# Optimization experiments

Hardware: AMD Instinct MI355X
Metric: run time of the kernel (lower is better)

## Reference

```python
import jax, jax.numpy as jnp
import numpy as np

N_QUBITS = 10
DIM = 1 << N_QUBITS  # 1024
N_OUT = 10


def _apply_ry(state, theta, q):
    # RY(theta) on qubit q; state: [B, 2^n] real (circuit is real-valued)
    B = state.shape[0]
    left = 1 << q
    right = 1 << (N_QUBITS - q - 1)
    s = state.reshape(B, left, 2, right)
    c = jnp.cos(theta / 2)
    sn = jnp.sin(theta / 2)
    s0 = c * s[:, :, 0] - sn * s[:, :, 1]
    s1 = sn * s[:, :, 0] + c * s[:, :, 1]
    return jnp.stack([s0, s1], axis=2).reshape(B, DIM)


def _apply_cnot(state, q):
    # CNOT with control q, target q+1 (adjacent, as in the source)
    B = state.shape[0]
    left = 1 << q
    right = 1 << (N_QUBITS - q - 2)
    s = state.reshape(B, left, 2, 2, right)
    s = jnp.concatenate([s[:, :, :1], jnp.flip(s[:, :, 1:], axis=3)], axis=2)
    return s.reshape(B, DIM)


def _simulate(x, params):
    B = x.shape[0]
    depth = params.shape[0]
    # weights = pi * tanh(weights)
    w = jnp.pi * jnp.tanh(params)
    # AmplitudeEmbedding: pad 784 -> 1024 with zeros, L2-normalize
    xp = jnp.pad(x, ((0, 0), (0, DIM - x.shape[1])))
    state = xp / jnp.linalg.norm(xp, axis=1, keepdims=True)
    for l in range(depth):
        # CNot(0, n): pairs (0,1),(2,3),...; CNot(1, n): pairs (1,2),(3,4),...
        for start in (0, 1):
            for i in range(start, N_QUBITS - 1, 2):
                state = _apply_cnot(state, i)
        # Rotation(w): RY(w[i]) on each wire
        for i in range(N_QUBITS):
            state = _apply_ry(state, w[l, i], i)
    # Measure: expval(PauliZ(p)) for p in range(out)
    probs = (state * state).reshape((B,) + (2,) * N_QUBITS)
    outs = []
    for p in range(N_OUT):
        axes = tuple(k + 1 for k in range(N_QUBITS) if k != p)
        marg = probs.sum(axis=axes)  # [B, 2]
        outs.append(marg[:, 0] - marg[:, 1])
    return jnp.stack(outs, axis=1).astype(jnp.float32)  # [B, out]


def setup_inputs() -> dict:
    key = jax.random.key(0)
    k1, k2 = jax.random.split(key)
    x = jax.random.uniform(k1, (16384, 784), dtype=jnp.float32)
    params = jax.random.normal(k2, (8, 10), dtype=jnp.float32)
    return {"input": x, "params": params}


def reference(input, params):
    return _simulate(input, params)
```

## Files before the change

kernel.cpp:

```cpp
#include <hip/hip_runtime.h>
#include <math.h>


template<int CTRL>
__device__ __forceinline__ float dpp_mov(float x) {
  int i = __builtin_bit_cast(int, x);
  i = __builtin_amdgcn_update_dpp(i, i, CTRL, 0xf, 0xf, true);
  return __builtin_bit_cast(float, i);
}
__device__ __forceinline__ float xl1(float x) { return dpp_mov<0xB1>(x); }
__device__ __forceinline__ float xl2(float x) { return dpp_mov<0x4E>(x); }
__device__ __forceinline__ float xl8(float x) { return dpp_mov<0x128>(x); }
template<int PAT>
__device__ __forceinline__ float swz(float x) {
  int i = __builtin_amdgcn_ds_swizzle(__builtin_bit_cast(int, x), PAT);
  return __builtin_bit_cast(float, i);
}
__device__ __forceinline__ float xl4(float x)  { return swz<0x101F>(x); }
__device__ __forceinline__ float xl16(float x) { return swz<0x401F>(x); }
__device__ __forceinline__ float bperm(int addr, float x) {
  int i = __builtin_amdgcn_ds_bpermute(addr, __builtin_bit_cast(int, x));
  return __builtin_bit_cast(float, i);
}
__device__ __forceinline__ float red32(float x) {
  x += xl1(x); x += xl2(x); x += xl4(x); x += xl8(x); x += xl16(x); return x;
}

template<int M>
__device__ __forceinline__ void ry_reg(float* v, float c, float s) {
  #pragma unroll
  for (int r = 0; r < 32; ++r) {
    if ((r & M) == 0) {
      float s0 = v[r], s1 = v[r + M];
      v[r]     = fmaf(c, s0, -(s * s1));
      v[r + M] = fmaf(s, s0,  c * s1);
    }
  }
}

template<int L2>
__device__ __forceinline__ float tree_level(float* v) {
  float a = 0.f, b = 0.f;
  #pragma unroll
  for (int j = 0; j < L2; ++j) {
    float e = v[2 * j], o = v[2 * j + 1];
    if (j & 1) b += e - o; else a += e - o;
    v[j] = e + o;
  }
  return a + b;
}

__global__ __launch_bounds__(256, 6) void circuit_kernel(
    const float* __restrict__ x, const float* __restrict__ params,
    float* __restrict__ out) {
  __shared__ float csh[160];

  const int tid  = threadIdx.x;
  const int wv   = tid >> 6;
  const int lane = tid & 63;
  const int h    = lane >> 5;
  const int l5   = lane & 31;
  const long elem = (long)blockIdx.x * 8 + wv * 2 + h;

  if (tid < 80) {
    float th = 1.57079632679489662f * tanhf(params[tid]);
    csh[2 * tid]     = cosf(th);
    csh[2 * tid + 1] = sinf(th);
  }

  int m = l5 ^ ((l5 & 4) >> 1);
  m ^= (m & 16) >> 1;
  m ^= (m & 2) >> 1;
  m ^= (m & 8) >> 1;
  const int addrE = ((lane & 32) | m) << 2;
  const int addrO = addrE ^ 64;

  float v[32];
  const float* xb = x + elem * 784 + l5;
  #pragma unroll
  for (int k = 0; k < 24; ++k) v[k] = xb[k * 32];
  v[24] = (l5 < 16) ? xb[768] : 0.f;
  #pragma unroll
  for (int k = 25; k < 32; ++k) v[k] = 0.f;

  float nn = 0.f;
  #pragma unroll
  for (int k = 0; k < 25; ++k) nn = fmaf(v[k], v[k], nn);
  nn = red32(nn);
  float scl = 1.0f / sqrtf(nn);
  #pragma unroll
  for (int k = 0; k < 25; ++k) v[k] *= scl;

  __syncthreads();

  #pragma unroll
  for (int l = 0; l < 8; ++l) {
    #pragma unroll
    for (int r = 0; r < 32; ++r) if ((r & 24) == 16) { float t = v[r]; v[r] = v[r + 8]; v[r + 8] = t; }
    #pragma unroll
    for (int r = 0; r < 32; ++r) if ((r & 6) == 4) { float t = v[r]; v[r] = v[r + 2]; v[r + 2] = t; }

    #pragma unroll
    for (int r = 0; r < 32; r += 2) {
      v[r]     = bperm(addrE, v[r]);
      v[r + 1] = bperm(addrO, v[r + 1]);
    }

    #pragma unroll
    for (int r = 0; r < 32; ++r) if ((r & 12) == 8) { float t = v[r]; v[r] = v[r + 4]; v[r + 4] = t; }
    #pragma unroll
    for (int r = 0; r < 32; ++r) if ((r & 3) == 2) { float t = v[r]; v[r] = v[r + 1]; v[r + 1] = t; }

    const float* cl = &csh[l * 20];
    ry_reg<16>(v, cl[0],  cl[1]);
    ry_reg< 8>(v, cl[2],  cl[3]);
    ry_reg< 4>(v, cl[4],  cl[5]);
    ry_reg< 2>(v, cl[6],  cl[7]);
    ry_reg< 1>(v, cl[8],  cl[9]);
    {
      float c = cl[10], s = cl[11];
      float sn = (lane & 16) ? s : -s;
      #pragma unroll
      for (int r = 0; r < 32; ++r) { float p = xl16(v[r]); v[r] = fmaf(c, v[r], sn * p); }
    }
    {
      float c = cl[12], s = cl[13];
      float sn = (lane & 8) ? s : -s;
      #pragma unroll
      for (int r = 0; r < 32; ++r) { float p = xl8(v[r]); v[r] = fmaf(c, v[r], sn * p); }
    }
    {
      float c = cl[14], s = cl[15];
      float sn = (lane & 4) ? s : -s;
      #pragma unroll
      for (int r = 0; r < 32; ++r) { float p = xl4(v[r]); v[r] = fmaf(c, v[r], sn * p); }
    }
    {
      float c = cl[16], s = cl[17];
      float sn = (lane & 2) ? s : -s;
      #pragma unroll
      for (int r = 0; r < 32; ++r) { float p = xl2(v[r]); v[r] = fmaf(c, v[r], sn * p); }
    }
    {
      float c = cl[18], s = cl[19];
      float sn = (lane & 1) ? s : -s;
      #pragma unroll
      for (int r = 0; r < 32; ++r) { float p = xl1(v[r]); v[r] = fmaf(c, v[r], sn * p); }
    }
  }

  float z[10];
  #pragma unroll
  for (int r = 0; r < 32; ++r) v[r] *= v[r];
  z[4] = red32(tree_level<16>(v));
  z[3] = red32(tree_level< 8>(v));
  z[2] = red32(tree_level< 4>(v));
  z[1] = red32(tree_level< 2>(v));
  z[0] = red32(tree_level< 1>(v));
  float W = v[0];
  { float u = W + xl1(W); u += xl2(u); u += xl4(u); u += xl8(u);  float t = u - xl16(u); z[5] = (lane & 16) ? -t : t; }
  { float u = W + xl1(W); u += xl2(u); u += xl4(u); u += xl16(u); float t = u - xl8(u);  z[6] = (lane & 8)  ? -t : t; }
  { float u = W + xl1(W); u += xl2(u); u += xl8(u); u += xl16(u); float t = u - xl4(u);  z[7] = (lane & 4)  ? -t : t; }
  { float u = W + xl1(W); u += xl4(u); u += xl8(u); u += xl16(u); float t = u - xl2(u);  z[8] = (lane & 2)  ? -t : t; }
  { float u = W + xl2(W); u += xl4(u); u += xl8(u); u += xl16(u); float t = u - xl1(u);  z[9] = (lane & 1)  ? -t : t; }

  float o = z[0];
  #pragma unroll
  for (int j = 1; j < 10; ++j) o = (l5 == j) ? z[j] : o;
  if (l5 < 10) out[elem * 10 + l5] = o;
}

extern "C" void kernel_launch(void* const* d_in, const int* in_sizes, int n_in,
                              void* d_out, int out_size, void* d_ws, size_t ws_size,
                              hipStream_t stream) {
  const float* x      = (const float*)d_in[0];
  const float* params = (const float*)d_in[1];
  float* out          = (float*)d_out;
  (void)d_ws; (void)ws_size; (void)in_sizes; (void)n_in; (void)out_size;
  circuit_kernel<<<2048, 256, 0, stream>>>(x, params, out);
}
```

Before: 73.84 us.

## Pack state into float2 vectors for packed FMA and defer normalization

```diff
diff --git a/kernel.cpp b/kernel.cpp
--- a/kernel.cpp
+++ b/kernel.cpp
@@ -1,6 +1,8 @@
 #include <hip/hip_runtime.h>
 #include <math.h>
 
+
+typedef float v2f __attribute__((ext_vector_type(2)));
 
 template<int CTRL>
 __device__ __forceinline__ float dpp_mov(float x) {
@@ -26,26 +28,14 @@
   x += xl1(x); x += xl2(x); x += xl4(x); x += xl8(x); x += xl16(x); return x;
 }
 
-template<int M>
-__device__ __forceinline__ void ry_reg(float* v, float c, float s) {
-  #pragma unroll
-  for (int r = 0; r < 32; ++r) {
-    if ((r & M) == 0) {
-      float s0 = v[r], s1 = v[r + M];
-      v[r]     = fmaf(c, s0, -(s * s1));
-      v[r + M] = fmaf(s, s0,  c * s1);
-    }
-  }
-}
-
 template<int L2>
-__device__ __forceinline__ float tree_level(float* v) {
+__device__ __forceinline__ float tree_level(float* t) {
   float a = 0.f, b = 0.f;
   #pragma unroll
   for (int j = 0; j < L2; ++j) {
-    float e = v[2 * j], o = v[2 * j + 1];
+    float e = t[2 * j], o = t[2 * j + 1];
     if (j & 1) b += e - o; else a += e - o;
-    v[j] = e + o;
+    t[j] = e + o;
   }
   return a + b;
 }
@@ -75,89 +65,134 @@
   const int addrE = ((lane & 32) | m) << 2;
   const int addrO = addrE ^ 64;
 
-  float v[32];
+  v2f w[16];
   const float* xb = x + elem * 784 + l5;
   #pragma unroll
-  for (int k = 0; k < 24; ++k) v[k] = xb[k * 32];
-  v[24] = (l5 < 16) ? xb[768] : 0.f;
-  #pragma unroll
-  for (int k = 25; k < 32; ++k) v[k] = 0.f;
-
-  float nn = 0.f;
-  #pragma unroll
-  for (int k = 0; k < 25; ++k) nn = fmaf(v[k], v[k], nn);
-  nn = red32(nn);
-  float scl = 1.0f / sqrtf(nn);
-  #pragma unroll
-  for (int k = 0; k < 25; ++k) v[k] *= scl;
+  for (int u = 0; u < 12; ++u) {
+    w[u].x = xb[u * 64];
+    w[u].y = xb[u * 64 + 32];
+  }
+  w[12].x = (l5 < 16) ? xb[768] : 0.f;
+  w[12].y = 0.f;
+  #pragma unroll
+  for (int u = 13; u < 16; ++u) w[u] = (v2f){0.f, 0.f};
+
+  v2f acc = {0.f, 0.f};
+  #pragma unroll
+  for (int u = 0; u < 13; ++u) acc += w[u] * w[u];
+  float nn  = red32(acc.x + acc.y);
+  float inv = 1.0f / nn;
 
   __syncthreads();
 
   #pragma unroll
   for (int l = 0; l < 8; ++l) {
-    #pragma unroll
-    for (int r = 0; r < 32; ++r) if ((r & 24) == 16) { float t = v[r]; v[r] = v[r + 8]; v[r + 8] = t; }
-    #pragma unroll
-    for (int r = 0; r < 32; ++r) if ((r & 6) == 4) { float t = v[r]; v[r] = v[r + 2]; v[r + 2] = t; }
-
-    #pragma unroll
-    for (int r = 0; r < 32; r += 2) {
-      v[r]     = bperm(addrE, v[r]);
-      v[r + 1] = bperm(addrO, v[r + 1]);
+    const float* cl = &csh[l * 20];
+
+    #pragma unroll
+    for (int u = 0; u < 16; ++u) if ((u & 12) == 8) { v2f t = w[u]; w[u] = w[u + 4]; w[u + 4] = t; }
+    #pragma unroll
+    for (int u = 0; u < 16; ++u) if ((u & 3) == 2) { v2f t = w[u]; w[u] = w[u + 1]; w[u + 1] = t; }
+
+    #pragma unroll
+    for (int u = 0; u < 16; ++u) {
+      w[u].x = bperm(addrE, w[u].x);
+      w[u].y = bperm(addrO, w[u].y);
     }
 
     #pragma unroll
-    for (int r = 0; r < 32; ++r) if ((r & 12) == 8) { float t = v[r]; v[r] = v[r + 4]; v[r + 4] = t; }
-    #pragma unroll
-    for (int r = 0; r < 32; ++r) if ((r & 3) == 2) { float t = v[r]; v[r] = v[r + 1]; v[r + 1] = t; }
-
-    const float* cl = &csh[l * 20];
-    ry_reg<16>(v, cl[0],  cl[1]);
-    ry_reg< 8>(v, cl[2],  cl[3]);
-    ry_reg< 4>(v, cl[4],  cl[5]);
-    ry_reg< 2>(v, cl[6],  cl[7]);
-    ry_reg< 1>(v, cl[8],  cl[9]);
-    {
-      float c = cl[10], s = cl[11];
-      float sn = (lane & 16) ? s : -s;
-      #pragma unroll
-      for (int r = 0; r < 32; ++r) { float p = xl16(v[r]); v[r] = fmaf(c, v[r], sn * p); }
-    }
-    {
-      float c = cl[12], s = cl[13];
-      float sn = (lane & 8) ? s : -s;
-      #pragma unroll
-      for (int r = 0; r < 32; ++r) { float p = xl8(v[r]); v[r] = fmaf(c, v[r], sn * p); }
-    }
-    {
-      float c = cl[14], s = cl[15];
-      float sn = (lane & 4) ? s : -s;
-      #pragma unroll
-      for (int r = 0; r < 32; ++r) { float p = xl4(v[r]); v[r] = fmaf(c, v[r], sn * p); }
-    }
-    {
-      float c = cl[16], s = cl[17];
-      float sn = (lane & 2) ? s : -s;
-      #pragma unroll
-      for (int r = 0; r < 32; ++r) { float p = xl2(v[r]); v[r] = fmaf(c, v[r], sn * p); }
-    }
-    {
-      float c = cl[18], s = cl[19];
-      float sn = (lane & 1) ? s : -s;
-      #pragma unroll
-      for (int r = 0; r < 32; ++r) { float p = xl1(v[r]); v[r] = fmaf(c, v[r], sn * p); }
-    }
-  }
-
+    for (int u = 0; u < 16; ++u) if ((u & 6) == 4) { v2f t = w[u]; w[u] = w[u + 2]; w[u + 2] = t; }
+    #pragma unroll
+    for (int u = 1; u < 16; u += 2) w[u] = __builtin_shufflevector(w[u], w[u], 1, 0);
+
+    { v2f cc = {cl[0], cl[0]}, ss = {cl[1], cl[1]};
+      #pragma unroll
+      for (int u = 0; u < 16; ++u) if ((u & 8) == 0) {
+        v2f a = w[u], b = w[u + 8];
+        w[u] = cc * a - ss * b;  w[u + 8] = ss * a + cc * b;
+      } }
+    { v2f cc = {cl[2], cl[2]}, ss = {cl[3], cl[3]};
+      #pragma unroll
+      for (int u = 0; u < 16; ++u) if ((u & 4) == 0) {
+        v2f a = w[u], b = w[u + 4];
+        w[u] = cc * a - ss * b;  w[u + 4] = ss * a + cc * b;
+      } }
+    { v2f cc = {cl[4], cl[4]}, ss = {cl[5], cl[5]};
+      #pragma unroll
+      for (int u = 0; u < 16; ++u) if ((u & 2) == 0) {
+        v2f a = w[u], b = w[u + 2];
+        w[u] = cc * a - ss * b;  w[u + 2] = ss * a + cc * b;
+      } }
+    { v2f cc = {cl[6], cl[6]}, ss = {cl[7], cl[7]};
+      #pragma unroll
+      for (int u = 0; u < 16; ++u) if ((u & 1) == 0) {
+        v2f a = w[u], b = w[u + 1];
+        w[u] = cc * a - ss * b;  w[u + 1] = ss * a + cc * b;
+      } }
+
+    { v2f A = {cl[8], cl[9]}, B = {-cl[9], cl[8]};
+      #pragma unroll
+      for (int u = 0; u < 16; ++u) {
+        v2f xx = __builtin_shufflevector(w[u], w[u], 0, 0);
+        v2f yy = __builtin_shufflevector(w[u], w[u], 1, 1);
+        w[u] = A * xx + B * yy;
+      } }
+
+    { float sn = (lane & 16) ? cl[11] : -cl[11];
+      v2f cc = {cl[10], cl[10]}, ssn = {sn, sn};
+      #pragma unroll
+      for (int u = 0; u < 16; ++u) {
+        v2f p = { xl16(w[u].x), xl16(w[u].y) };
+        w[u] = cc * w[u] + ssn * p;
+      } }
+    { float sn = (lane & 8) ? cl[13] : -cl[13];
+      v2f cc = {cl[12], cl[12]}, ssn = {sn, sn};
+      #pragma unroll
+      for (int u = 0; u < 16; ++u) {
+        v2f p = { xl8(w[u].x), xl8(w[u].y) };
+        w[u] = cc * w[u] + ssn * p;
+      } }
+    { float sn = (lane & 4) ? cl[15] : -cl[15];
+      v2f cc = {cl[14], cl[14]}, ssn = {sn, sn};
+      #pragma unroll
+      for (int u = 0; u < 16; ++u) {
+        v2f p = { xl4(w[u].x), xl4(w[u].y) };
+        w[u] = cc * w[u] + ssn * p;
+      } }
+    { float sn = (lane & 2) ? cl[17] : -cl[17];
+      v2f cc = {cl[16], cl[16]}, ssn = {sn, sn};
+      #pragma unroll
+      for (int u = 0; u < 16; ++u) {
+        v2f p = { xl2(w[u].x), xl2(w[u].y) };
+        w[u] = cc * w[u] + ssn * p;
+      } }
+    { float sn = (lane & 1) ? cl[19] : -cl[19];
+      v2f cc = {cl[18], cl[18]}, ssn = {sn, sn};
+      #pragma unroll
+      for (int u = 0; u < 16; ++u) {
+        v2f p = { xl1(w[u].x), xl1(w[u].y) };
+        w[u] = cc * w[u] + ssn * p;
+      } }
+  }
+
+  #pragma unroll
+  for (int u = 0; u < 16; ++u) w[u] *= w[u];
+
+  float t16[16];
+  float a0 = 0.f, a1 = 0.f;
+  #pragma unroll
+  for (int u = 0; u < 16; ++u) {
+    float d = w[u].x - w[u].y;
+    if (u & 1) a1 += d; else a0 += d;
+    t16[u] = w[u].x + w[u].y;
+  }
   float z[10];
-  #pragma unroll
-  for (int r = 0; r < 32; ++r) v[r] *= v[r];
-  z[4] = red32(tree_level<16>(v));
-  z[3] = red32(tree_level< 8>(v));
-  z[2] = red32(tree_level< 4>(v));
-  z[1] = red32(tree_level< 2>(v));
-  z[0] = red32(tree_level< 1>(v));
-  float W = v[0];
+  z[4] = red32(a0 + a1);
+  z[3] = red32(tree_level<8>(t16));
+  z[2] = red32(tree_level<4>(t16));
+  z[1] = red32(tree_level<2>(t16));
+  z[0] = red32(tree_level<1>(t16));
+  float W = t16[0];
   { float u = W + xl1(W); u += xl2(u); u += xl4(u); u += xl8(u);  float t = u - xl16(u); z[5] = (lane & 16) ? -t : t; }
   { float u = W + xl1(W); u += xl2(u); u += xl4(u); u += xl16(u); float t = u - xl8(u);  z[6] = (lane & 8)  ? -t : t; }
   { float u = W + xl1(W); u += xl2(u); u += xl8(u); u += xl16(u); float t = u - xl4(u);  z[7] = (lane & 4)  ? -t : t; }
@@ -167,7 +202,7 @@
   float o = z[0];
   #pragma unroll
   for (int j = 1; j < 10; ++j) o = (l5 == j) ? z[j] : o;
-  if (l5 < 10) out[elem * 10 + l5] = o;
+  if (l5 < 10) out[elem * 10 + l5] = o * inv;
 }
 
 extern "C" void kernel_launch(void* const* d_in, const int* in_sizes, int n_in,
```

New measurement: 75.61 us. +2.4%, slower.

## Factor RY cosines out as per-layer scale and use tangent-form rotations

Applied to the files above, without the earlier changes.

```diff
diff --git a/kernel.cpp b/kernel.cpp
--- a/kernel.cpp
+++ b/kernel.cpp
@@ -11,6 +11,9 @@
 __device__ __forceinline__ float xl1(float x) { return dpp_mov<0xB1>(x); }
 __device__ __forceinline__ float xl2(float x) { return dpp_mov<0x4E>(x); }
 __device__ __forceinline__ float xl8(float x) { return dpp_mov<0x128>(x); }
+__device__ __forceinline__ float xl4d(float x) {
+  return dpp_mov<0x141>(dpp_mov<0x1B>(x));
+}
 template<int PAT>
 __device__ __forceinline__ float swz(float x) {
   int i = __builtin_amdgcn_ds_swizzle(__builtin_bit_cast(int, x), PAT);
@@ -27,13 +30,13 @@
 }
 
 template<int M>
-__device__ __forceinline__ void ry_reg(float* v, float c, float s) {
+__device__ __forceinline__ void ry_reg_t(float* v, float t) {
   #pragma unroll
   for (int r = 0; r < 32; ++r) {
     if ((r & M) == 0) {
-      float s0 = v[r], s1 = v[r + M];
-      v[r]     = fmaf(c, s0, -(s * s1));
-      v[r + M] = fmaf(s, s0,  c * s1);
+      float a = v[r], b = v[r + M];
+      v[r]     = fmaf(-t, b, a);
+      v[r + M] = fmaf( t, a, b);
     }
   }
 }
@@ -53,7 +56,7 @@
 __global__ __launch_bounds__(256, 6) void circuit_kernel(
     const float* __restrict__ x, const float* __restrict__ params,
     float* __restrict__ out) {
-  __shared__ float csh[160];
+  __shared__ float csh[168];
 
   const int tid  = threadIdx.x;
   const int wv   = tid >> 6;
@@ -64,8 +67,9 @@
 
   if (tid < 80) {
     float th = 1.57079632679489662f * tanhf(params[tid]);
-    csh[2 * tid]     = cosf(th);
-    csh[2 * tid + 1] = sinf(th);
+    float c = cosf(th), s = sinf(th);
+    csh[2 * tid]     = s / c;
+    csh[2 * tid + 1] = c;
   }
 
   int m = l5 ^ ((l5 & 4) >> 1);
@@ -87,14 +91,21 @@
   #pragma unroll
   for (int k = 0; k < 25; ++k) nn = fmaf(v[k], v[k], nn);
   nn = red32(nn);
-  float scl = 1.0f / sqrtf(nn);
-  #pragma unroll
-  for (int k = 0; k < 25; ++k) v[k] *= scl;
+  float inv = 1.0f / nn;
 
+  __syncthreads();
+  if (tid < 8) {
+    float P = 1.f;
+    #pragma unroll
+    for (int q = 0; q < 10; ++q) P *= csh[tid * 20 + 2 * q + 1];
+    csh[160 + tid] = P;
+  }
   __syncthreads();
 
   #pragma unroll
   for (int l = 0; l < 8; ++l) {
+    const float* cl = &csh[l * 20];
+
     #pragma unroll
     for (int r = 0; r < 32; ++r) if ((r & 24) == 16) { float t = v[r]; v[r] = v[r + 8]; v[r + 8] = t; }
     #pragma unroll
@@ -111,42 +122,30 @@
     #pragma unroll
     for (int r = 0; r < 32; ++r) if ((r & 3) == 2) { float t = v[r]; v[r] = v[r + 1]; v[r + 1] = t; }
 
-    const float* cl = &csh[l * 20];
-    ry_reg<16>(v, cl[0],  cl[1]);
-    ry_reg< 8>(v, cl[2],  cl[3]);
-    ry_reg< 4>(v, cl[4],  cl[5]);
-    ry_reg< 2>(v, cl[6],  cl[7]);
-    ry_reg< 1>(v, cl[8],  cl[9]);
-    {
-      float c = cl[10], s = cl[11];
-      float sn = (lane & 16) ? s : -s;
+    ry_reg_t<16>(v, cl[0]);
+    ry_reg_t< 8>(v, cl[2]);
+    ry_reg_t< 4>(v, cl[4]);
+    ry_reg_t< 2>(v, cl[6]);
+    ry_reg_t< 1>(v, cl[8]);
+    { float t = cl[10]; float tsn = (lane & 16) ? t : -t;
       #pragma unroll
-      for (int r = 0; r < 32; ++r) { float p = xl16(v[r]); v[r] = fmaf(c, v[r], sn * p); }
-    }
-    {
-      float c = cl[12], s = cl[13];
-      float sn = (lane & 8) ? s : -s;
+      for (int r = 0; r < 32; ++r) v[r] = fmaf(tsn, xl16(v[r]), v[r]); }
+    { float t = cl[12]; float tsn = (lane & 8) ? t : -t;
       #pragma unroll
-      for (int r = 0; r < 32; ++r) { float p = xl8(v[r]); v[r] = fmaf(c, v[r], sn * p); }
-    }
-    {
-      float c = cl[14], s = cl[15];
-      float sn = (lane & 4) ? s : -s;
+      for (int r = 0; r < 32; ++r) v[r] = fmaf(tsn, xl8(v[r]), v[r]); }
+    { float t = cl[14]; float tsn = (lane & 4) ? t : -t;
       #pragma unroll
-      for (int r = 0; r < 32; ++r) { float p = xl4(v[r]); v[r] = fmaf(c, v[r], sn * p); }
-    }
-    {
-      float c = cl[16], s = cl[17];
-      float sn = (lane & 2) ? s : -s;
+      for (int r = 0; r < 32; ++r) v[r] = fmaf(tsn, xl4d(v[r]), v[r]); }
+    { float t = cl[16]; float tsn = (lane & 2) ? t : -t;
       #pragma unroll
-      for (int r = 0; r < 32; ++r) { float p = xl2(v[r]); v[r] = fmaf(c, v[r], sn * p); }
-    }
-    {
-      float c = cl[18], s = cl[19];
-      float sn = (lane & 1) ? s : -s;
+      for (int r = 0; r < 32; ++r) v[r] = fmaf(tsn, xl2(v[r]), v[r]); }
+    { float t = cl[18]; float tsn = (lane & 1) ? t : -t;
       #pragma unroll
-      for (int r = 0; r < 32; ++r) { float p = xl1(v[r]); v[r] = fmaf(c, v[r], sn * p); }
-    }
+      for (int r = 0; r < 32; ++r) v[r] = fmaf(tsn, xl1(v[r]), v[r]); }
+
+    { float ls = csh[160 + l];
+      #pragma unroll
+      for (int r = 0; r < 32; ++r) v[r] *= ls; }
   }
 
   float z[10];
@@ -167,7 +166,7 @@
   float o = z[0];
   #pragma unroll
   for (int j = 1; j < 10; ++j) o = (l5 == j) ? z[j] : o;
-  if (l5 < 10) out[elem * 10 + l5] = o;
+  if (l5 < 10) out[elem * 10 + l5] = o * inv;
 }
 
 extern "C" void kernel_launch(void* const* d_in, const int* in_sizes, int n_in,
```

After: 61.61 us. 16.6% less time.
